# Performance work log

Hardware: AMD Instinct MI355X
Metric: run time of the kernel (lower is better)

Reference implementation:

```python
import jax, jax.numpy as jnp
import numpy as np

V = 50257  # bittensor.__vocab_size__
E, B, K, D = 16, 256, 4097, 1024
HID = [512, 256, 128]
EPS = 1e-6


def setup_inputs() -> dict:
    key = jax.random.key(0)
    ks = jax.random.split(key, 20)
    endpoint_emb = jax.random.normal(ks[0], (E, B, D), dtype=jnp.float32)
    # prediction: [...,0]=prob, [...,1]=token index; indices unique per (e,b) row
    stride = V // K  # 12 -> max index K*stride < V
    offs = jax.random.randint(ks[1], (E, B, K), 0, stride)
    idx = jnp.arange(K, dtype=jnp.int32)[None, None, :] * stride + offs
    probs = jax.random.uniform(ks[2], (E, B, K), dtype=jnp.float32)
    prediction = jnp.stack([probs, idx.astype(jnp.float32)], axis=-1)
    # MLP params: Linear + LayerNorm (annotated-transformer style) per hidden dim
    params = {}
    d_in = D
    for i, h in enumerate(HID, start=1):
        params[f'W{i}'] = jax.random.normal(ks[2 + 2 * i], (d_in, h), dtype=jnp.float32) / np.sqrt(d_in)
        params[f'b{i}'] = jnp.zeros((h,), jnp.float32)
        params[f'g{i}'] = jnp.ones((h,), jnp.float32)
        params[f'be{i}'] = jnp.zeros((h,), jnp.float32)
        d_in = h
    params['Wout'] = jax.random.normal(ks[19], (d_in, 1), dtype=jnp.float32) / np.sqrt(d_in)
    params['bout'] = jnp.zeros((1,), jnp.float32)
    return dict(endpoint_emb=endpoint_emb, prediction=prediction, **params)


def _layernorm(x, g, b):
    mu = x.mean(-1, keepdims=True)
    sd = jnp.std(x, axis=-1, ddof=1, keepdims=True)  # torch.std default: unbiased
    return g * (x - mu) / (sd + EPS) + b


def reference(endpoint_emb, prediction, W1, b1, g1, be1, W2, b2, g2, be2, W3, b3, g3, be3, Wout, bout):
    h = endpoint_emb  # [E, B, D]
    for W, b, g, be in ((W1, b1, g1, be1), (W2, b2, g2, be2), (W3, b3, g3, be3)):
        h = _layernorm(jax.nn.elu(h @ W + b), g, be)
    # routing: [E, B], softmax over last axis (as in the original squeeze(-1))
    routing = jax.nn.softmax((h @ Wout + bout).squeeze(-1), axis=-1)
    # mix_response: per-expert scatter of probs into vocab slots, weighted sum.
    probs = prediction[:, :, :-1, 0]                    # [E, B, K-1]
    idx = prediction[:, :, :-1, 1].astype(jnp.int32)    # [E, B, K-1]
    vals = routing[:, :, None] * probs                  # [E, B, K-1]
    batch_ids = jnp.broadcast_to(jnp.arange(B)[None, :, None], idx.shape)
    mixed = jnp.zeros((B, V), jnp.float32).at[batch_ids, idx].add(vals)
    out = jnp.zeros((B, V + 1, 2), jnp.float32)
    out = out.at[:, :V, 0].set(mixed)
    out = out.at[:, :V, 1].set(jnp.arange(V, dtype=jnp.float32))
    out = out.at[:, V, 1].set(-1.0)  # last row = [0, -1]
    return out
```

## Files before the change

### kernel.cpp

```cpp
#include <hip/hip_runtime.h>

#define EPS 1e-6f

typedef __bf16 bf16x8 __attribute__((ext_vector_type(8)));
typedef float  fx4 __attribute__((ext_vector_type(4)));
typedef float  fx2 __attribute__((ext_vector_type(2)));

__global__ __launch_bounds__(256) void transpose_all(const float* __restrict__ W1,
                                                     const float* __restrict__ W2,
                                                     const float* __restrict__ W3,
                                                     __bf16* __restrict__ W1T,
                                                     __bf16* __restrict__ W2T,
                                                     __bf16* __restrict__ W3T) {
    int blk = blockIdx.x;
    const float* W; __bf16* WT; int Kd, Nd, t0;
    if (blk < 2048)      { W = W1; WT = W1T; Kd = 1024; Nd = 512; t0 = blk * 256; }
    else if (blk < 2560) { W = W2; WT = W2T; Kd = 512;  Nd = 256; t0 = (blk - 2048) * 256; }
    else                 { W = W3; WT = W3T; Kd = 256;  Nd = 128; t0 = (blk - 2560) * 256; }
    int t = t0 + threadIdx.x;
    int n = t / Kd, k = t % Kd;
    WT[t] = (__bf16)W[(size_t)k * Nd + n];
}

__global__ __launch_bounds__(256) void mlp_fused(const float* __restrict__ emb,
    const __bf16* __restrict__ W1T, const __bf16* __restrict__ W2T, const __bf16* __restrict__ W3T,
    const float* __restrict__ b1, const float* __restrict__ g1, const float* __restrict__ be1,
    const float* __restrict__ b2, const float* __restrict__ g2, const float* __restrict__ be2,
    const float* __restrict__ b3, const float* __restrict__ g3, const float* __restrict__ be3,
    const float* __restrict__ Wout, const float* __restrict__ bout,
    float* __restrict__ logits) {

    __shared__ __align__(16) __bf16 As[16][40];
    __shared__ __align__(16) __bf16 Bs[512][40];
    __shared__ __align__(16) __bf16 H1s[16][520];
    __shared__ __align__(16) __bf16 H2s[16][264];
    __shared__ float red[4][16][2];

    const int tid  = threadIdx.x;
    const int w    = tid >> 6, lane = tid & 63;
    const int quad = lane >> 4, col = lane & 15;
    const int m0   = blockIdx.x * 16;

    fx4 acc[8];
#pragma unroll
    for (int nt = 0; nt < 8; nt++) acc[nt] = fx4{0, 0, 0, 0};

    for (int k0 = 0; k0 < 1024; k0 += 32) {
        bf16x8 av;
        if (tid < 64) {
            const float* p = emb + (size_t)(m0 + (tid >> 2)) * 1024 + k0 + (tid & 3) * 8;
            float4 a0 = *(const float4*)p;
            float4 a1 = *(const float4*)(p + 4);
            av[0] = (__bf16)a0.x; av[1] = (__bf16)a0.y; av[2] = (__bf16)a0.z; av[3] = (__bf16)a0.w;
            av[4] = (__bf16)a1.x; av[5] = (__bf16)a1.y; av[6] = (__bf16)a1.z; av[7] = (__bf16)a1.w;
        }
        bf16x8 bv[8];
#pragma unroll
        for (int j = 0; j < 8; j++) {
            int c = tid + 256 * j;
            bv[j] = *(const bf16x8*)(W1T + (size_t)(c >> 2) * 1024 + k0 + (c & 3) * 8);
        }
        __syncthreads();
        if (tid < 64) *(bf16x8*)&As[tid >> 2][(tid & 3) * 8] = av;
#pragma unroll
        for (int j = 0; j < 8; j++) {
            int c = tid + 256 * j;
            *(bf16x8*)&Bs[c >> 2][(c & 3) * 8] = bv[j];
        }
        __syncthreads();
        bf16x8 a = *(const bf16x8*)&As[col][quad * 8];
#pragma unroll
        for (int nt = 0; nt < 8; nt++) {
            bf16x8 b = *(const bf16x8*)&Bs[w * 128 + nt * 16 + col][quad * 8];
            acc[nt] = __builtin_amdgcn_mfma_f32_16x16x32_bf16(a, b, acc[nt], 0, 0, 0);
        }
    }
    {
        float s[4] = {0,0,0,0}, s2[4] = {0,0,0,0};
#pragma unroll
        for (int nt = 0; nt < 8; nt++) {
            float bn = b1[w * 128 + nt * 16 + col];
#pragma unroll
            for (int r = 0; r < 4; r++) {
                float v = acc[nt][r] + bn;
                v = v > 0.f ? v : expm1f(v);
                acc[nt][r] = v;
                s[r] += v; s2[r] += v * v;
            }
        }
#pragma unroll
        for (int r = 0; r < 4; r++)
#pragma unroll
            for (int off = 1; off < 16; off <<= 1) {
                s[r]  += __shfl_xor(s[r], off);
                s2[r] += __shfl_xor(s2[r], off);
            }
        if (col == 0) {
#pragma unroll
            for (int r = 0; r < 4; r++) {
                red[w][quad * 4 + r][0] = s[r];
                red[w][quad * 4 + r][1] = s2[r];
            }
        }
        __syncthreads();
        float mu[4], inv[4];
#pragma unroll
        for (int r = 0; r < 4; r++) {
            int row = quad * 4 + r;
            float ss  = red[0][row][0] + red[1][row][0] + red[2][row][0] + red[3][row][0];
            float ss2 = red[0][row][1] + red[1][row][1] + red[2][row][1] + red[3][row][1];
            float m   = ss / 512.f;
            float var = (ss2 - 512.f * m * m) / 511.f;
            var = fmaxf(var, 0.f);
            mu[r] = m; inv[r] = 1.f / (sqrtf(var) + EPS);
        }
#pragma unroll
        for (int nt = 0; nt < 8; nt++) {
            int n = w * 128 + nt * 16 + col;
            float gg = g1[n], bb = be1[n];
#pragma unroll
            for (int r = 0; r < 4; r++)
                H1s[quad * 4 + r][n] = (__bf16)((acc[nt][r] - mu[r]) * inv[r] * gg + bb);
        }
    }

    fx4 acc2[4];
#pragma unroll
    for (int nt = 0; nt < 4; nt++) acc2[nt] = fx4{0, 0, 0, 0};

    for (int k0 = 0; k0 < 512; k0 += 32) {
        bf16x8 bv[4];
#pragma unroll
        for (int j = 0; j < 4; j++) {
            int c = tid + 256 * j;
            bv[j] = *(const bf16x8*)(W2T + (size_t)(c >> 2) * 512 + k0 + (c & 3) * 8);
        }
        __syncthreads();
#pragma unroll
        for (int j = 0; j < 4; j++) {
            int c = tid + 256 * j;
            *(bf16x8*)&Bs[c >> 2][(c & 3) * 8] = bv[j];
        }
        __syncthreads();
        bf16x8 a = *(const bf16x8*)&H1s[col][k0 + quad * 8];
#pragma unroll
        for (int nt = 0; nt < 4; nt++) {
            bf16x8 b = *(const bf16x8*)&Bs[w * 64 + nt * 16 + col][quad * 8];
            acc2[nt] = __builtin_amdgcn_mfma_f32_16x16x32_bf16(a, b, acc2[nt], 0, 0, 0);
        }
    }
    {
        float s[4] = {0,0,0,0}, s2[4] = {0,0,0,0};
#pragma unroll
        for (int nt = 0; nt < 4; nt++) {
            float bn = b2[w * 64 + nt * 16 + col];
#pragma unroll
            for (int r = 0; r < 4; r++) {
                float v = acc2[nt][r] + bn;
                v = v > 0.f ? v : expm1f(v);
                acc2[nt][r] = v;
                s[r] += v; s2[r] += v * v;
            }
        }
#pragma unroll
        for (int r = 0; r < 4; r++)
#pragma unroll
            for (int off = 1; off < 16; off <<= 1) {
                s[r]  += __shfl_xor(s[r], off);
                s2[r] += __shfl_xor(s2[r], off);
            }
        if (col == 0) {
#pragma unroll
            for (int r = 0; r < 4; r++) {
                red[w][quad * 4 + r][0] = s[r];
                red[w][quad * 4 + r][1] = s2[r];
            }
        }
        __syncthreads();
        float mu[4], inv[4];
#pragma unroll
        for (int r = 0; r < 4; r++) {
            int row = quad * 4 + r;
            float ss  = red[0][row][0] + red[1][row][0] + red[2][row][0] + red[3][row][0];
            float ss2 = red[0][row][1] + red[1][row][1] + red[2][row][1] + red[3][row][1];
            float m   = ss / 256.f;
            float var = (ss2 - 256.f * m * m) / 255.f;
            var = fmaxf(var, 0.f);
            mu[r] = m; inv[r] = 1.f / (sqrtf(var) + EPS);
        }
#pragma unroll
        for (int nt = 0; nt < 4; nt++) {
            int n = w * 64 + nt * 16 + col;
            float gg = g2[n], bb = be2[n];
#pragma unroll
            for (int r = 0; r < 4; r++)
                H2s[quad * 4 + r][n] = (__bf16)((acc2[nt][r] - mu[r]) * inv[r] * gg + bb);
        }
    }

    fx4 acc3[2];
#pragma unroll
    for (int nt = 0; nt < 2; nt++) acc3[nt] = fx4{0, 0, 0, 0};

    for (int k0 = 0; k0 < 256; k0 += 32) {
        bf16x8 bv[2];
#pragma unroll
        for (int j = 0; j < 2; j++) {
            int c = tid + 256 * j;
            bv[j] = *(const bf16x8*)(W3T + (size_t)(c >> 2) * 256 + k0 + (c & 3) * 8);
        }
        __syncthreads();
#pragma unroll
        for (int j = 0; j < 2; j++) {
            int c = tid + 256 * j;
            *(bf16x8*)&Bs[c >> 2][(c & 3) * 8] = bv[j];
        }
        __syncthreads();
        bf16x8 a = *(const bf16x8*)&H2s[col][k0 + quad * 8];
#pragma unroll
        for (int nt = 0; nt < 2; nt++) {
            bf16x8 b = *(const bf16x8*)&Bs[w * 32 + nt * 16 + col][quad * 8];
            acc3[nt] = __builtin_amdgcn_mfma_f32_16x16x32_bf16(a, b, acc3[nt], 0, 0, 0);
        }
    }
    {
        float s[4] = {0,0,0,0}, s2[4] = {0,0,0,0};
#pragma unroll
        for (int nt = 0; nt < 2; nt++) {
            float bn = b3[w * 32 + nt * 16 + col];
#pragma unroll
            for (int r = 0; r < 4; r++) {
                float v = acc3[nt][r] + bn;
                v = v > 0.f ? v : expm1f(v);
                acc3[nt][r] = v;
                s[r] += v; s2[r] += v * v;
            }
        }
#pragma unroll
        for (int r = 0; r < 4; r++)
#pragma unroll
            for (int off = 1; off < 16; off <<= 1) {
                s[r]  += __shfl_xor(s[r], off);
                s2[r] += __shfl_xor(s2[r], off);
            }
        if (col == 0) {
#pragma unroll
            for (int r = 0; r < 4; r++) {
                red[w][quad * 4 + r][0] = s[r];
                red[w][quad * 4 + r][1] = s2[r];
            }
        }
        __syncthreads();
        float mu[4], inv[4];
#pragma unroll
        for (int r = 0; r < 4; r++) {
            int row = quad * 4 + r;
            float ss  = red[0][row][0] + red[1][row][0] + red[2][row][0] + red[3][row][0];
            float ss2 = red[0][row][1] + red[1][row][1] + red[2][row][1] + red[3][row][1];
            float m   = ss / 128.f;
            float var = (ss2 - 128.f * m * m) / 127.f;
            var = fmaxf(var, 0.f);
            mu[r] = m; inv[r] = 1.f / (sqrtf(var) + EPS);
        }
        float lg[4] = {0,0,0,0};
#pragma unroll
        for (int nt = 0; nt < 2; nt++) {
            int n = w * 32 + nt * 16 + col;
            float gg = g3[n], bb = be3[n], wo = Wout[n];
#pragma unroll
            for (int r = 0; r < 4; r++)
                lg[r] += ((acc3[nt][r] - mu[r]) * inv[r] * gg + bb) * wo;
        }
#pragma unroll
        for (int r = 0; r < 4; r++)
#pragma unroll
            for (int off = 1; off < 16; off <<= 1) lg[r] += __shfl_xor(lg[r], off);
        __syncthreads();
        if (col == 0) {
#pragma unroll
            for (int r = 0; r < 4; r++) red[w][quad * 4 + r][0] = lg[r];
        }
        __syncthreads();
        if (tid < 16)
            logits[m0 + tid] = red[0][tid][0] + red[1][tid][0] + red[2][tid][0] + red[3][tid][0] + bout[0];
    }
}

__global__ __launch_bounds__(256) void routing_kernel(const float* __restrict__ logits,
                                                      float* __restrict__ routing) {
    int e = blockIdx.x;
    int tid = threadIdx.x;
    float l = logits[e * 256 + tid];
    __shared__ float sh[4];
    float m = l;
#pragma unroll
    for (int off = 32; off >= 1; off >>= 1) m = fmaxf(m, __shfl_down(m, off, 64));
    if ((tid & 63) == 0) sh[tid >> 6] = m;
    __syncthreads();
    m = fmaxf(fmaxf(sh[0], sh[1]), fmaxf(sh[2], sh[3]));
    __syncthreads();
    float ex = __expf(l - m);
    float ssum = ex;
#pragma unroll
    for (int off = 32; off >= 1; off >>= 1) ssum += __shfl_down(ssum, off, 64);
    if ((tid & 63) == 0) sh[tid >> 6] = ssum;
    __syncthreads();
    ssum = sh[0] + sh[1] + sh[2] + sh[3];
    routing[e * 256 + tid] = ex / ssum;
}

#define VV 50257
#define KK 4097

__global__ __launch_bounds__(256) void scatter_kernel(const fx2* __restrict__ pred,
                                                      const float* __restrict__ routing,
                                                      float* __restrict__ out) {
    __shared__ float vals[3072];
    __shared__ float rsh[16];
    int b   = blockIdx.y;
    int tid = threadIdx.x;
    int kb  = blockIdx.x * 256 + tid;
    if (tid < 16) rsh[tid] = routing[tid * 256 + b];
#pragma unroll
    for (int i = 0; i < 12; i++) vals[tid + i * 256] = 0.f;
    __syncthreads();

    if (kb < 4096) {
        float bins[12];
#pragma unroll
        for (int r = 0; r < 12; r++) bins[r] = 0.f;
#pragma unroll
        for (int e = 0; e < 16; e++) {
            fx2 p = __builtin_nontemporal_load(pred + (size_t)(e * 256 + b) * KK + kb);
            int r = (int)p[1] - kb * 12;
            float val = rsh[e] * p[0];
#pragma unroll
            for (int rr = 0; rr < 12; rr++)
                if (rr == r) bins[rr] += val;
        }
#pragma unroll
        for (int r = 0; r < 12; r++) vals[tid * 12 + r] = bins[r];
    }
    __syncthreads();

    int v0 = blockIdx.x * 3072;
    int nv = min(3072, (VV + 1) - v0);
    int nf = nv * 2;
    float* orow = out + (size_t)b * (2 * (VV + 1));
    for (int f = tid * 4; f < nf; f += 1024) {
        int rv = f >> 1;
        int v  = v0 + rv;
        fx4 wv;
        wv[0] = vals[rv];
        wv[1] = (float)v;
        if (v + 1 == VV) { wv[2] = 0.f; wv[3] = -1.f; }
        else             { wv[2] = vals[rv + 1]; wv[3] = (float)(v + 1); }
        __builtin_nontemporal_store(wv, (fx4*)(orow + (size_t)v * 2));
    }
}


extern "C" void kernel_launch(void* const* d_in, const int* in_sizes, int n_in,
                              void* d_out, int out_size, void* d_ws, size_t ws_size,
                              hipStream_t stream) {
    const float* emb  = (const float*)d_in[0];
    const fx2*   pred = (const fx2*)d_in[1];
    const float* W1 = (const float*)d_in[2];
    const float* b1 = (const float*)d_in[3];
    const float* g1 = (const float*)d_in[4];
    const float* be1 = (const float*)d_in[5];
    const float* W2 = (const float*)d_in[6];
    const float* b2 = (const float*)d_in[7];
    const float* g2 = (const float*)d_in[8];
    const float* be2 = (const float*)d_in[9];
    const float* W3 = (const float*)d_in[10];
    const float* b3 = (const float*)d_in[11];
    const float* g3 = (const float*)d_in[12];
    const float* be3 = (const float*)d_in[13];
    const float* Wout = (const float*)d_in[14];
    const float* bout = (const float*)d_in[15];

    char* ws = (char*)d_ws;
    __bf16* W1T = (__bf16*)ws;    ws += (size_t)512 * 1024 * 2;
    __bf16* W2T = (__bf16*)ws;    ws += (size_t)256 * 512 * 2;
    __bf16* W3T = (__bf16*)ws;    ws += (size_t)128 * 256 * 2;
    float* logits  = (float*)ws;  ws += 4096 * 4;
    float* routing = (float*)ws;  ws += 4096 * 4;

    transpose_all<<<2688, 256, 0, stream>>>(W1, W2, W3, W1T, W2T, W3T);

    mlp_fused<<<256, 256, 0, stream>>>(emb, W1T, W2T, W3T,
                                       b1, g1, be1, b2, g2, be2, b3, g3, be3,
                                       Wout, bout, logits);

    routing_kernel<<<16, 256, 0, stream>>>(logits, routing);
    scatter_kernel<<<dim3(17, 256), 256, 0, stream>>>(pred, routing, (float*)d_out);
}
```

Baseline: 317.3 us.

## Tile weight transpose via LDS, prefetch GEMM operands, pad scatter LDS bins

The weight transpose now stages 32x64 tiles through padded shared memory, so both global reads and bf16 writes are coalesced instead of strided. The three MLP GEMM loops load the next K-slice into registers while the current slice is being consumed, overlapping global latency with MFMA work. The scatter kernel pads its per-thread bin array to a stride of 13 to avoid LDS bank conflicts, at the cost of a division by 12 when reading bins back. Holding the prefetch buffers adds register pressure.

```diff
diff --git a/kernel.cpp b/kernel.cpp
--- a/kernel.cpp
+++ b/kernel.cpp
@@ -3,6 +3,7 @@
 #define EPS 1e-6f
 
 typedef __bf16 bf16x8 __attribute__((ext_vector_type(8)));
+typedef __bf16 bf16x4 __attribute__((ext_vector_type(4)));
 typedef float  fx4 __attribute__((ext_vector_type(4)));
 typedef float  fx2 __attribute__((ext_vector_type(2)));
 
@@ -12,14 +13,34 @@
                                                      __bf16* __restrict__ W1T,
                                                      __bf16* __restrict__ W2T,
                                                      __bf16* __restrict__ W3T) {
+    __shared__ float tile[32][65];
     int blk = blockIdx.x;
-    const float* W; __bf16* WT; int Kd, Nd, t0;
-    if (blk < 2048)      { W = W1; WT = W1T; Kd = 1024; Nd = 512; t0 = blk * 256; }
-    else if (blk < 2560) { W = W2; WT = W2T; Kd = 512;  Nd = 256; t0 = (blk - 2048) * 256; }
-    else                 { W = W3; WT = W3T; Kd = 256;  Nd = 128; t0 = (blk - 2560) * 256; }
-    int t = t0 + threadIdx.x;
-    int n = t / Kd, k = t % Kd;
-    WT[t] = (__bf16)W[(size_t)k * Nd + n];
+    const float* W; __bf16* WT; int Kd, Nd, t;
+    if (blk < 256)      { W = W1; WT = W1T; Kd = 1024; Nd = 512; t = blk; }
+    else if (blk < 320) { W = W2; WT = W2T; Kd = 512;  Nd = 256; t = blk - 256; }
+    else                { W = W3; WT = W3T; Kd = 256;  Nd = 128; t = blk - 320; }
+    int nkt = Kd / 32;
+    int k0 = (t % nkt) * 32, n0 = (t / nkt) * 64;
+
+    int tid = threadIdx.x;
+    int rk = tid >> 4, rn4 = (tid & 15) * 4;
+#pragma unroll
+    for (int p = 0; p < 32; p += 16) {
+        float4 v = *(const float4*)(W + (size_t)(k0 + rk + p) * Nd + n0 + rn4);
+        tile[rk + p][rn4]     = v.x;
+        tile[rk + p][rn4 + 1] = v.y;
+        tile[rk + p][rn4 + 2] = v.z;
+        tile[rk + p][rn4 + 3] = v.w;
+    }
+    __syncthreads();
+    int wn = tid >> 3, wk4 = (tid & 7) * 4;
+#pragma unroll
+    for (int q = 0; q < 64; q += 32) {
+        bf16x4 o;
+#pragma unroll
+        for (int j = 0; j < 4; j++) o[j] = (__bf16)tile[wk4 + j][wn + q];
+        *(bf16x4*)(WT + (size_t)(n0 + wn + q) * Kd + k0 + wk4) = o;
+    }
 }
 
 __global__ __launch_bounds__(256) void mlp_fused(const float* __restrict__ emb,
@@ -45,27 +66,48 @@
 #pragma unroll
     for (int nt = 0; nt < 8; nt++) acc[nt] = fx4{0, 0, 0, 0};
 
+    float4 a0p, a1p;
+    bf16x8 bvp[8];
+    {
+        if (tid < 64) {
+            const float* p = emb + (size_t)(m0 + (tid >> 2)) * 1024 + (tid & 3) * 8;
+            a0p = *(const float4*)p;
+            a1p = *(const float4*)(p + 4);
+        }
+#pragma unroll
+        for (int j = 0; j < 8; j++) {
+            int c = tid + 256 * j;
+            bvp[j] = *(const bf16x8*)(W1T + (size_t)(c >> 2) * 1024 + (c & 3) * 8);
+        }
+    }
     for (int k0 = 0; k0 < 1024; k0 += 32) {
-        bf16x8 av;
+        float4 a0 = a0p, a1 = a1p;
+        bf16x8 bv[8];
+#pragma unroll
+        for (int j = 0; j < 8; j++) bv[j] = bvp[j];
+        __syncthreads();
         if (tid < 64) {
-            const float* p = emb + (size_t)(m0 + (tid >> 2)) * 1024 + k0 + (tid & 3) * 8;
-            float4 a0 = *(const float4*)p;
-            float4 a1 = *(const float4*)(p + 4);
+            bf16x8 av;
             av[0] = (__bf16)a0.x; av[1] = (__bf16)a0.y; av[2] = (__bf16)a0.z; av[3] = (__bf16)a0.w;
             av[4] = (__bf16)a1.x; av[5] = (__bf16)a1.y; av[6] = (__bf16)a1.z; av[7] = (__bf16)a1.w;
-        }
-        bf16x8 bv[8];
-#pragma unroll
-        for (int j = 0; j < 8; j++) {
-            int c = tid + 256 * j;
-            bv[j] = *(const bf16x8*)(W1T + (size_t)(c >> 2) * 1024 + k0 + (c & 3) * 8);
-        }
-        __syncthreads();
-        if (tid < 64) *(bf16x8*)&As[tid >> 2][(tid & 3) * 8] = av;
+            *(bf16x8*)&As[tid >> 2][(tid & 3) * 8] = av;
+        }
 #pragma unroll
         for (int j = 0; j < 8; j++) {
             int c = tid + 256 * j;
             *(bf16x8*)&Bs[c >> 2][(c & 3) * 8] = bv[j];
+        }
+        if (k0 + 32 < 1024) {
+            if (tid < 64) {
+                const float* p = emb + (size_t)(m0 + (tid >> 2)) * 1024 + k0 + 32 + (tid & 3) * 8;
+                a0p = *(const float4*)p;
+                a1p = *(const float4*)(p + 4);
+            }
+#pragma unroll
+            for (int j = 0; j < 8; j++) {
+                int c = tid + 256 * j;
+                bvp[j] = *(const bf16x8*)(W1T + (size_t)(c >> 2) * 1024 + k0 + 32 + (c & 3) * 8);
+            }
         }
         __syncthreads();
         bf16x8 a = *(const bf16x8*)&As[col][quad * 8];
@@ -128,18 +170,28 @@
 #pragma unroll
     for (int nt = 0; nt < 4; nt++) acc2[nt] = fx4{0, 0, 0, 0};
 
+    bf16x8 bvp2[4];
+#pragma unroll
+    for (int j = 0; j < 4; j++) {
+        int c = tid + 256 * j;
+        bvp2[j] = *(const bf16x8*)(W2T + (size_t)(c >> 2) * 512 + (c & 3) * 8);
+    }
     for (int k0 = 0; k0 < 512; k0 += 32) {
         bf16x8 bv[4];
 #pragma unroll
-        for (int j = 0; j < 4; j++) {
-            int c = tid + 256 * j;
-            bv[j] = *(const bf16x8*)(W2T + (size_t)(c >> 2) * 512 + k0 + (c & 3) * 8);
-        }
+        for (int j = 0; j < 4; j++) bv[j] = bvp2[j];
         __syncthreads();
 #pragma unroll
         for (int j = 0; j < 4; j++) {
             int c = tid + 256 * j;
             *(bf16x8*)&Bs[c >> 2][(c & 3) * 8] = bv[j];
+        }
+        if (k0 + 32 < 512) {
+#pragma unroll
+            for (int j = 0; j < 4; j++) {
+                int c = tid + 256 * j;
+                bvp2[j] = *(const bf16x8*)(W2T + (size_t)(c >> 2) * 512 + k0 + 32 + (c & 3) * 8);
+            }
         }
         __syncthreads();
         bf16x8 a = *(const bf16x8*)&H1s[col][k0 + quad * 8];
@@ -202,18 +254,28 @@
 #pragma unroll
     for (int nt = 0; nt < 2; nt++) acc3[nt] = fx4{0, 0, 0, 0};
 
+    bf16x8 bvp3[2];
+#pragma unroll
+    for (int j = 0; j < 2; j++) {
+        int c = tid + 256 * j;
+        bvp3[j] = *(const bf16x8*)(W3T + (size_t)(c >> 2) * 256 + (c & 3) * 8);
+    }
     for (int k0 = 0; k0 < 256; k0 += 32) {
         bf16x8 bv[2];
 #pragma unroll
-        for (int j = 0; j < 2; j++) {
-            int c = tid + 256 * j;
-            bv[j] = *(const bf16x8*)(W3T + (size_t)(c >> 2) * 256 + k0 + (c & 3) * 8);
-        }
+        for (int j = 0; j < 2; j++) bv[j] = bvp3[j];
         __syncthreads();
 #pragma unroll
         for (int j = 0; j < 2; j++) {
             int c = tid + 256 * j;
             *(bf16x8*)&Bs[c >> 2][(c & 3) * 8] = bv[j];
+        }
+        if (k0 + 32 < 256) {
+#pragma unroll
+            for (int j = 0; j < 2; j++) {
+                int c = tid + 256 * j;
+                bvp3[j] = *(const bf16x8*)(W3T + (size_t)(c >> 2) * 256 + k0 + 32 + (c & 3) * 8);
+            }
         }
         __syncthreads();
         bf16x8 a = *(const bf16x8*)&H2s[col][k0 + quad * 8];
@@ -315,14 +377,14 @@
 __global__ __launch_bounds__(256) void scatter_kernel(const fx2* __restrict__ pred,
                                                       const float* __restrict__ routing,
                                                       float* __restrict__ out) {
-    __shared__ float vals[3072];
+    __shared__ float vals[256 * 13];
     __shared__ float rsh[16];
     int b   = blockIdx.y;
     int tid = threadIdx.x;
     int kb  = blockIdx.x * 256 + tid;
     if (tid < 16) rsh[tid] = routing[tid * 256 + b];
 #pragma unroll
-    for (int i = 0; i < 12; i++) vals[tid + i * 256] = 0.f;
+    for (int i = 0; i < 13; i++) vals[tid + i * 256] = 0.f;
     __syncthreads();
 
     if (kb < 4096) {
@@ -339,7 +401,7 @@
                 if (rr == r) bins[rr] += val;
         }
 #pragma unroll
-        for (int r = 0; r < 12; r++) vals[tid * 12 + r] = bins[r];
+        for (int r = 0; r < 12; r++) vals[tid * 13 + r] = bins[r];
     }
     __syncthreads();
 
@@ -350,11 +412,13 @@
     for (int f = tid * 4; f < nf; f += 1024) {
         int rv = f >> 1;
         int v  = v0 + rv;
+        int kl0 = rv / 12,       r0 = rv - kl0 * 12;
+        int kl1 = (rv + 1) / 12, r1 = (rv + 1) - kl1 * 12;
         fx4 wv;
-        wv[0] = vals[rv];
+        wv[0] = vals[kl0 * 13 + r0];
         wv[1] = (float)v;
         if (v + 1 == VV) { wv[2] = 0.f; wv[3] = -1.f; }
-        else             { wv[2] = vals[rv + 1]; wv[3] = (float)(v + 1); }
+        else             { wv[2] = vals[kl1 * 13 + r1]; wv[3] = (float)(v + 1); }
         __builtin_nontemporal_store(wv, (fx4*)(orow + (size_t)v * 2));
     }
 }
@@ -387,7 +451,7 @@
     float* logits  = (float*)ws;  ws += 4096 * 4;
     float* routing = (float*)ws;  ws += 4096 * 4;
 
-    transpose_all<<<2688, 256, 0, stream>>>(W1, W2, W3, W1T, W2T, W3T);
+    transpose_all<<<336, 256, 0, stream>>>(W1, W2, W3, W1T, W2T, W3T);
 
     mlp_fused<<<256, 256, 0, stream>>>(emb, W1T, W2T, W3T,
                                        b1, g1, be1, b2, g2, be2, b3, g3, be3,
```

Result: faster. 296.9 us (-6.4%).
